# Performance work log

Hardware: AMD Instinct MI355X
Metric: run time of the kernel (lower is better)

## Reference

```python
import jax, jax.numpy as jnp
import numpy as np

# Block-sparse layout constants (must match init_kwargs):
BS = 64       # block_size (= block_m = block_n)
NB = 64       # number of blocks per side -> max_seqlen = 4096
LOCAL = 8     # causal sliding window of 8 blocks
GLOBAL = 1    # 1 global (attention-sink) block


def _layout():
    """Build padded per-row block column indices and the token-level mask.

    Mirrors dkernel semantics: block (i, j) participates iff sparse_pattern[i, j] == 1,
    and within participating blocks a per-token causal mask (k_pos <= q_pos) is applied
    (dkernel applies causal masking on diagonal blocks; off-diagonal lower blocks pass
    the causal test trivially, so pattern & causal is exact).
    """
    i = np.arange(NB)[:, None]
    j = np.arange(NB)[None, :]
    pat = (j <= i) & (((i - j) < LOCAL) | (j < GLOBAL))  # [NB, NB] bool
    max_nnz = int(pat.sum(-1).max())                      # = LOCAL + GLOBAL = 9
    col = np.zeros((NB, max_nnz), np.int32)
    valid = np.zeros((NB, max_nnz), bool)
    for r in range(NB):
        idx = np.nonzero(pat[r])[0]
        col[r, :len(idx)] = idx
        valid[r, :len(idx)] = True
    # token positions
    qpos = np.arange(NB)[:, None] * BS + np.arange(BS)[None, :]                    # [NB, BS]
    kpos = (col[:, :, None] * BS + np.arange(BS)[None, None, :]).reshape(NB, -1)   # [NB, max_nnz*BS]
    vmask = np.repeat(valid, BS, axis=1)                                           # [NB, max_nnz*BS]
    mask = vmask[:, None, :] & (kpos[:, None, :] <= qpos[:, :, None])              # [NB, BS, max_nnz*BS]
    return col, mask

_COL, _MASK = _layout()


def setup_inputs() -> dict:
    key = jax.random.key(0)
    kq, kk, kv = jax.random.split(key, 3)
    B, S, H, D = 2, 4096, 16, 128
    q = jax.random.normal(kq, (B, S, H, D), dtype=jnp.float32)
    k = jax.random.normal(kk, (B, S, H, D), dtype=jnp.float32)
    v = jax.random.normal(kv, (B, S, H, D), dtype=jnp.float32)
    return {"q": q, "k": k, "v": v}


def reference(q, k, v):
    B, S, H, D = q.shape
    sm_scale = 1.0 / np.sqrt(float(D))  # default sm_scale in forward()
    # -> [B, H, NB, BS, D]
    qb = q.reshape(B, NB, BS, H, D).transpose(0, 3, 1, 2, 4)
    kb = k.reshape(B, NB, BS, H, D).transpose(0, 3, 1, 2, 4)
    vb = v.reshape(B, NB, BS, H, D).transpose(0, 3, 1, 2, 4)
    col = jnp.asarray(_COL)                              # [NB, max_nnz]
    # gather the kv blocks each q-block attends to: [B, H, NB, max_nnz*BS, D]
    kg = kb[:, :, col].reshape(B, H, NB, -1, D)
    vg = vb[:, :, col].reshape(B, H, NB, -1, D)
    # block-sparse scores: [B, H, NB, BS, max_nnz*BS]
    s = jnp.einsum('bhnqd,bhnkd->bhnqk', qb, kg) * sm_scale
    s = jnp.where(jnp.asarray(_MASK)[None, None], s, -jnp.inf)
    p = jax.nn.softmax(s, axis=-1)
    o = jnp.einsum('bhnqk,bhnkd->bhnqd', p, vg)          # [B, H, NB, BS, D]
    return o.transpose(0, 2, 3, 1, 4).reshape(B, S, H, D)
```

## Files before the change

### kernel.cpp

```cpp
#include <hip/hip_runtime.h>
#include <hip/hip_bf16.h>


typedef __bf16 bf16_t;
typedef bf16_t bf16x8 __attribute__((ext_vector_type(8)));
typedef bf16_t bf16x4 __attribute__((ext_vector_type(4)));
typedef float f32x4 __attribute__((ext_vector_type(4)));
typedef uint32_t u32x4 __attribute__((ext_vector_type(4)));

#define BSZ 64
#define DIM 128
#define NH 16
#define SEQ 4096
#define ROWSTRIDE (NH * DIM)

__device__ __forceinline__ uint32_t kb_swz(uint32_t A) {
    return A ^ (((A >> 8) & 7u) << 4);
}
__device__ __forceinline__ uint32_t vt_swz(uint32_t A) {
    return A ^ (((A >> 9) & 7u) << 4) ^ (((A >> 8) & 1u) << 6);
}

__global__ __launch_bounds__(256) void sparse_attn_kernel(
    const float* __restrict__ q, const float* __restrict__ k,
    const float* __restrict__ v, float* __restrict__ out)
{
    __shared__ __align__(16) bf16_t Kb[BSZ * DIM];
    __shared__ __align__(16) bf16_t Vt[DIM * BSZ];

    const int L  = ((blockIdx.x & 7) << 8) | (blockIdx.x >> 3);
    const int qi = L & 63;
    const int h  = (L >> 6) & 15;
    const int b  = L >> 10;

    const int tid  = threadIdx.x;
    const int wave = tid >> 6;
    const int lane = tid & 63;
    const int lr = lane & 15;
    const int lk = lane >> 4;
    const int k0 = lk * 8;

    const int sc4 = tid & 31;
    const int sr  = tid >> 5;

    const float scale2 = 0.12751649736230476f;

    const size_t bh_off = ((size_t)b * SEQ * NH + (size_t)h) * DIM;
    const float* kbh = k + bh_off;
    const float* vbh = v + bh_off;

    bf16x8 qf[4];
    {
        const float* qrow = q + bh_off + (size_t)(qi * 64 + wave * 16 + lr) * ROWSTRIDE;
        #pragma unroll
        for (int kk = 0; kk < 4; ++kk) {
            const float4 a0 = *(const float4*)(qrow + 32 * kk + k0);
            const float4 a1 = *(const float4*)(qrow + 32 * kk + k0 + 4);
            bf16x8 f;
            f[0] = (bf16_t)(a0.x * scale2); f[1] = (bf16_t)(a0.y * scale2);
            f[2] = (bf16_t)(a0.z * scale2); f[3] = (bf16_t)(a0.w * scale2);
            f[4] = (bf16_t)(a1.x * scale2); f[5] = (bf16_t)(a1.y * scale2);
            f[6] = (bf16_t)(a1.z * scale2); f[7] = (bf16_t)(a1.w * scale2);
            qf[kk] = f;
        }
    }

    f32x4 oacc[8];
    #pragma unroll
    for (int n = 0; n < 8; ++n) oacc[n] = (f32x4){0.f, 0.f, 0.f, 0.f};
    float mrun = -3.0e38f, lrun = 0.f;

    const int qrow_local = wave * 16 + lr;
    const int nnz = (qi < 8) ? (qi + 1) : 9;

    float4 kreg[8];
    float4 vreg[8];

    #define LOAD_K(jb)                                                            \
    {                                                                             \
        const float* kb_ = kbh + (size_t)((jb) * 64) * ROWSTRIDE + 4 * sc4;       \
        _Pragma("unroll")                                                         \
        for (int i = 0; i < 8; ++i)                                               \
            kreg[i] = *(const float4*)(kb_ + (size_t)(8 * i + sr) * ROWSTRIDE);   \
    }
    #define LOAD_V(jb)                                                            \
    {                                                                             \
        const float* vb_ = vbh + (size_t)((jb) * 64) * ROWSTRIDE + 4 * sc4;       \
        _Pragma("unroll")                                                         \
        for (int T = 0; T < 2; ++T)                                               \
            _Pragma("unroll")                                                     \
            for (int i = 0; i < 4; ++i)                                           \
                vreg[T * 4 + i] = *(const float4*)(vb_ +                          \
                    (size_t)(4 * (sr + 8 * T) + i) * ROWSTRIDE);                  \
    }

    LOAD_K(0);

    for (int t = 0; t < nnz; ++t) {
        const int j = (qi < 8) ? t : ((t == 0) ? 0 : (qi - 8 + t));

        LOAD_V(j);

        #pragma unroll
        for (int i = 0; i < 8; ++i) {
            const float4 t4 = kreg[i];
            bf16x4 c = {(bf16_t)t4.x, (bf16_t)t4.y, (bf16_t)t4.z, (bf16_t)t4.w};
            const uint32_t A = kb_swz((uint32_t)((8 * i + sr) * 256 + 8 * sc4));
            *(bf16x4*)((char*)Kb + A) = c;
        }
        __syncthreads();

        f32x4 sacc[4];
        __builtin_amdgcn_s_setprio(1);
        #pragma unroll
        for (int n = 0; n < 4; ++n) {
            f32x4 a = (f32x4){0.f, 0.f, 0.f, 0.f};
            #pragma unroll
            for (int kk = 0; kk < 4; ++kk) {
                const uint32_t A = kb_swz((uint32_t)((16 * n + lr) * 256 + 64 * kk + 16 * lk));
                bf16x8 kf = *(const bf16x8*)((const char*)Kb + A);
                a = __builtin_amdgcn_mfma_f32_16x16x32_bf16(kf, qf[kk], a, 0, 0, 0);
            }
            sacc[n] = a;
        }
        __builtin_amdgcn_s_setprio(0);

        #pragma unroll
        for (int T = 0; T < 2; ++T) {
            #pragma unroll
            for (int j2 = 0; j2 < 4; ++j2) {
                const int d = 4 * sc4 + j2;
                bf16x4 c = {(bf16_t)((const float*)&vreg[T * 4 + 0])[j2],
                            (bf16_t)((const float*)&vreg[T * 4 + 1])[j2],
                            (bf16_t)((const float*)&vreg[T * 4 + 2])[j2],
                            (bf16_t)((const float*)&vreg[T * 4 + 3])[j2]};
                const uint32_t A = vt_swz((uint32_t)(d * 128 + 8 * (sr + 8 * T)));
                *(bf16x4*)((char*)Vt + A) = c;
            }
        }

        if (j == qi) {
            #pragma unroll
            for (int n = 0; n < 4; ++n)
                #pragma unroll
                for (int r = 0; r < 4; ++r) {
                    if (16 * n + 4 * lk + r > qrow_local) sacc[n][r] = -1.0e30f;
                }
        }
        float vmax = -3.0e38f;
        #pragma unroll
        for (int n = 0; n < 4; ++n)
            #pragma unroll
            for (int r = 0; r < 4; ++r) vmax = fmaxf(vmax, sacc[n][r]);
        vmax = fmaxf(vmax, __shfl_xor(vmax, 16));
        vmax = fmaxf(vmax, __shfl_xor(vmax, 32));

        if (!__all(vmax - mrun <= 8.0f)) {
            const float mnew = fmaxf(mrun, vmax);
            const float alpha = exp2f(mrun - mnew);
            mrun = mnew;
            lrun *= alpha;
            float av[4];
            #pragma unroll
            for (int r = 0; r < 4; ++r) av[r] = __shfl(alpha, 4 * lk + r);
            #pragma unroll
            for (int n = 0; n < 8; ++n)
                #pragma unroll
                for (int r = 0; r < 4; ++r) oacc[n][r] *= av[r];
        }
        uint32_t ch[8];
        #pragma unroll
        for (int n = 0; n < 4; ++n) {
            float p0 = exp2f(sacc[n][0] - mrun);
            float p1 = exp2f(sacc[n][1] - mrun);
            float p2 = exp2f(sacc[n][2] - mrun);
            float p3 = exp2f(sacc[n][3] - mrun);
            lrun += (p0 + p1) + (p2 + p3);
            bf16x4 c4 = {(bf16_t)p0, (bf16_t)p1, (bf16_t)p2, (bf16_t)p3};
            uint32_t* cw = (uint32_t*)&c4;
            ch[2 * n]     = cw[0];
            ch[2 * n + 1] = cw[1];
        }

        bf16x8 paf[2];
        {
            const int s0 = lr + 32 * (lk & 1);
            const bool hi = (lk & 2) != 0;
            #pragma unroll
            for (int kk = 0; kk < 2; ++kk) {
                uint32_t res[4];
                #pragma unroll
                for (int u = 0; u < 2; ++u) {
                    const uint32_t a0 = (uint32_t)__shfl((int)ch[4 * kk + u],     s0);
                    const uint32_t b0 = (uint32_t)__shfl((int)ch[4 * kk + 2 + u], s0);
                    const uint32_t a1 = (uint32_t)__shfl((int)ch[4 * kk + u],     s0 + 16);
                    const uint32_t b1 = (uint32_t)__shfl((int)ch[4 * kk + 2 + u], s0 + 16);
                    res[u]     = hi ? b0 : a0;
                    res[2 + u] = hi ? b1 : a1;
                }
                u32x4 tv = {res[0], res[1], res[2], res[3]};
                paf[kk] = *(bf16x8*)&tv;
            }
        }

        if (t + 1 < nnz) {
            const int jn = (qi < 8) ? (t + 1) : (qi - 8 + t + 1);
            LOAD_K(jn);
        }
        __syncthreads();

        __builtin_amdgcn_s_setprio(1);
        #pragma unroll
        for (int n = 0; n < 8; ++n) {
            f32x4 a = oacc[n];
            #pragma unroll
            for (int kk = 0; kk < 2; ++kk) {
                const uint32_t Av = vt_swz((uint32_t)((16 * n + lr) * 128 + 64 * kk + 16 * lk));
                bf16x8 vf = *(const bf16x8*)((const char*)Vt + Av);
                a = __builtin_amdgcn_mfma_f32_16x16x32_bf16(paf[kk], vf, a, 0, 0, 0);
            }
            oacc[n] = a;
        }
        __builtin_amdgcn_s_setprio(0);
    }

    float lrtot = lrun;
    lrtot += __shfl_xor(lrtot, 16);
    lrtot += __shfl_xor(lrtot, 32);
    float* obase = out + bh_off + (size_t)(qi * 64 + wave * 16) * ROWSTRIDE;
    #pragma unroll
    for (int r = 0; r < 4; ++r) {
        const float inv = 1.0f / __shfl(lrtot, 4 * lk + r);
        float* orow = obase + (size_t)(4 * lk + r) * ROWSTRIDE;
        #pragma unroll
        for (int n = 0; n < 8; ++n) {
            orow[16 * n + lr] = oacc[n][r] * inv;
        }
    }
}

extern "C" void kernel_launch(void* const* d_in, const int* in_sizes, int n_in,
                              void* d_out, int out_size, void* d_ws, size_t ws_size,
                              hipStream_t stream) {
    const float* q = (const float*)d_in[0];
    const float* k = (const float*)d_in[1];
    const float* v = (const float*)d_in[2];
    float* out = (float*)d_out;
    sparse_attn_kernel<<<dim3(2048), dim3(256), 0, stream>>>(q, k, v, out);
}
```

Measured before the change: 105.5 us.

## Process two adjacent query blocks per workgroup to share K/V tile loads

Each workgroup now handles a pair of consecutive query blocks, iterating over the union of their KV windows so each K/V block is loaded from global memory, converted to bf16 and staged in LDS once for both queries. The grid is halved and every MFMA step issues two independent chains. This cuts redundant fp32 K/V traffic and conversion work, but doubles accumulator registers, which may lower occupancy, and halves the number of workgroups available to fill the GPU. The V-transpose swizzle also gains an extra bit.

After: 163.5 us. 54.9% more time.

```diff
diff --git a/kernel.cpp b/kernel.cpp
--- a/kernel.cpp
+++ b/kernel.cpp
@@ -8,7 +8,6 @@
 typedef float f32x4 __attribute__((ext_vector_type(4)));
 typedef uint32_t u32x4 __attribute__((ext_vector_type(4)));
 
-#define BSZ 64
 #define DIM 128
 #define NH 16
 #define SEQ 4096
@@ -18,27 +17,49 @@
     return A ^ (((A >> 8) & 7u) << 4);
 }
 __device__ __forceinline__ uint32_t vt_swz(uint32_t A) {
-    return A ^ (((A >> 9) & 7u) << 4) ^ (((A >> 8) & 1u) << 6);
+    return A ^ (((A >> 9) & 7u) << 4) ^ (((A >> 8) & 1u) << 6) ^ (((A >> 12) & 1u) << 7);
+}
+
+__device__ __forceinline__ void exchange_paf(const uint32_t ch[8], int lr, int lk,
+                                             bf16x8 paf[2]) {
+    const int s0 = lr + 32 * (lk & 1);
+    const bool hi = (lk & 2) != 0;
+    #pragma unroll
+    for (int kk = 0; kk < 2; ++kk) {
+        uint32_t res[4];
+        #pragma unroll
+        for (int u = 0; u < 2; ++u) {
+            const uint32_t a0 = (uint32_t)__shfl((int)ch[4 * kk + u],     s0);
+            const uint32_t b0 = (uint32_t)__shfl((int)ch[4 * kk + 2 + u], s0);
+            const uint32_t a1 = (uint32_t)__shfl((int)ch[4 * kk + u],     s0 + 16);
+            const uint32_t b1 = (uint32_t)__shfl((int)ch[4 * kk + 2 + u], s0 + 16);
+            res[u]     = hi ? b0 : a0;
+            res[2 + u] = hi ? b1 : a1;
+        }
+        u32x4 tv = {res[0], res[1], res[2], res[3]};
+        paf[kk] = *(bf16x8*)&tv;
+    }
 }
 
 __global__ __launch_bounds__(256) void sparse_attn_kernel(
     const float* __restrict__ q, const float* __restrict__ k,
     const float* __restrict__ v, float* __restrict__ out)
 {
-    __shared__ __align__(16) bf16_t Kb[BSZ * DIM];
-    __shared__ __align__(16) bf16_t Vt[DIM * BSZ];
-
-    const int L  = ((blockIdx.x & 7) << 8) | (blockIdx.x >> 3);
-    const int qi = L & 63;
-    const int h  = (L >> 6) & 15;
-    const int b  = L >> 10;
+    __shared__ __align__(16) bf16_t Kb[64 * DIM];
+    __shared__ __align__(16) bf16_t Vt[DIM * 64];
+
+    const int L  = ((blockIdx.x & 7) << 7) | (blockIdx.x >> 3);
+    const int g  = L & 31;
+    const int h  = (L >> 5) & 15;
+    const int b  = L >> 9;
+    const int qiA = 2 * g;
+    const int qiB = 2 * g + 1;
 
     const int tid  = threadIdx.x;
     const int wave = tid >> 6;
     const int lane = tid & 63;
     const int lr = lane & 15;
     const int lk = lane >> 4;
-    const int k0 = lk * 8;
 
     const int sc4 = tid & 31;
     const int sr  = tid >> 5;
@@ -49,29 +70,36 @@
     const float* kbh = k + bh_off;
     const float* vbh = v + bh_off;
 
-    bf16x8 qf[4];
-    {
+    bf16x8 qfA[4], qfB[4];
+    #pragma unroll
+    for (int blk = 0; blk < 2; ++blk) {
+        const int qi = blk ? qiB : qiA;
         const float* qrow = q + bh_off + (size_t)(qi * 64 + wave * 16 + lr) * ROWSTRIDE;
         #pragma unroll
         for (int kk = 0; kk < 4; ++kk) {
-            const float4 a0 = *(const float4*)(qrow + 32 * kk + k0);
-            const float4 a1 = *(const float4*)(qrow + 32 * kk + k0 + 4);
+            const float4 a0 = *(const float4*)(qrow + 32 * kk + 8 * lk);
+            const float4 a1 = *(const float4*)(qrow + 32 * kk + 8 * lk + 4);
             bf16x8 f;
             f[0] = (bf16_t)(a0.x * scale2); f[1] = (bf16_t)(a0.y * scale2);
             f[2] = (bf16_t)(a0.z * scale2); f[3] = (bf16_t)(a0.w * scale2);
             f[4] = (bf16_t)(a1.x * scale2); f[5] = (bf16_t)(a1.y * scale2);
             f[6] = (bf16_t)(a1.z * scale2); f[7] = (bf16_t)(a1.w * scale2);
-            qf[kk] = f;
-        }
-    }
-
-    f32x4 oacc[8];
-    #pragma unroll
-    for (int n = 0; n < 8; ++n) oacc[n] = (f32x4){0.f, 0.f, 0.f, 0.f};
-    float mrun = -3.0e38f, lrun = 0.f;
-
+            if (blk) qfB[kk] = f; else qfA[kk] = f;
+        }
+    }
+
+    f32x4 oA[8], oB[8];
+    #pragma unroll
+    for (int n = 0; n < 8; ++n) {
+        oA[n] = (f32x4){0.f, 0.f, 0.f, 0.f};
+        oB[n] = (f32x4){0.f, 0.f, 0.f, 0.f};
+    }
+    float mrunA = -3.0e38f, lrunA = 0.f;
+    float mrunB = -3.0e38f, lrunB = 0.f;
     const int qrow_local = wave * 16 + lr;
-    const int nnz = (qi < 8) ? (qi + 1) : 9;
+
+    const int lo  = (2 * g - 7 > 1) ? (2 * g - 7) : 1;
+    const int nit = 2 * g + 3 - lo;
 
     float4 kreg[8];
     float4 vreg[8];
@@ -94,10 +122,57 @@
                     (size_t)(4 * (sr + 8 * T) + i) * ROWSTRIDE);                  \
     }
 
+    #define SOFTMAX_EXCH(sX, mrunX, lrunX, oX, pafX, diagX)                       \
+    {                                                                             \
+        if (diagX) {                                                              \
+            _Pragma("unroll")                                                     \
+            for (int n = 0; n < 4; ++n)                                           \
+                _Pragma("unroll")                                                 \
+                for (int r = 0; r < 4; ++r)                                       \
+                    if (16 * n + 4 * lk + r > qrow_local) sX[n][r] = -1.0e30f;    \
+        }                                                                         \
+        float vmax = -3.0e38f;                                                    \
+        _Pragma("unroll")                                                         \
+        for (int n = 0; n < 4; ++n)                                               \
+            _Pragma("unroll")                                                     \
+            for (int r = 0; r < 4; ++r) vmax = fmaxf(vmax, sX[n][r]);             \
+        vmax = fmaxf(vmax, __shfl_xor(vmax, 16));                                 \
+        vmax = fmaxf(vmax, __shfl_xor(vmax, 32));                                 \
+        if (!__all(vmax - mrunX <= 8.0f)) {                                       \
+            const float mnew = fmaxf(mrunX, vmax);                                \
+            const float alpha = exp2f(mrunX - mnew);                              \
+            mrunX = mnew;                                                         \
+            lrunX *= alpha;                                                       \
+            float av[4];                                                          \
+            _Pragma("unroll")                                                     \
+            for (int r = 0; r < 4; ++r) av[r] = __shfl(alpha, 4 * lk + r);        \
+            _Pragma("unroll")                                                     \
+            for (int n = 0; n < 8; ++n)                                           \
+                _Pragma("unroll")                                                 \
+                for (int r = 0; r < 4; ++r) oX[n][r] *= av[r];                    \
+        }                                                                         \
+        uint32_t ch[8];                                                           \
+        _Pragma("unroll")                                                         \
+        for (int n = 0; n < 4; ++n) {                                             \
+            float p0 = exp2f(sX[n][0] - mrunX);                                   \
+            float p1 = exp2f(sX[n][1] - mrunX);                                   \
+            float p2 = exp2f(sX[n][2] - mrunX);                                   \
+            float p3 = exp2f(sX[n][3] - mrunX);                                   \
+            lrunX += (p0 + p1) + (p2 + p3);                                       \
+            bf16x4 c4 = {(bf16_t)p0, (bf16_t)p1, (bf16_t)p2, (bf16_t)p3};         \
+            uint32_t* cw = (uint32_t*)&c4;                                        \
+            ch[2 * n]     = cw[0];                                                \
+            ch[2 * n + 1] = cw[1];                                                \
+        }                                                                         \
+        exchange_paf(ch, lr, lk, pafX);                                           \
+    }
+
     LOAD_K(0);
 
-    for (int t = 0; t < nnz; ++t) {
-        const int j = (qi < 8) ? t : ((t == 0) ? 0 : (qi - 8 + t));
+    for (int t = 0; t < nit; ++t) {
+        const int j = (t == 0) ? 0 : (lo + t - 1);
+        const bool actA = (j == 0) || (j >= qiA - 7 && j <= qiA);
+        const bool actB = (j == 0) || (j >= qiB - 7 && j <= qiB);
 
         LOAD_V(j);
 
@@ -110,18 +185,21 @@
         }
         __syncthreads();
 
-        f32x4 sacc[4];
+        f32x4 sA[4], sB[4];
         __builtin_amdgcn_s_setprio(1);
         #pragma unroll
         for (int n = 0; n < 4; ++n) {
             f32x4 a = (f32x4){0.f, 0.f, 0.f, 0.f};
+            f32x4 c = (f32x4){0.f, 0.f, 0.f, 0.f};
             #pragma unroll
             for (int kk = 0; kk < 4; ++kk) {
                 const uint32_t A = kb_swz((uint32_t)((16 * n + lr) * 256 + 64 * kk + 16 * lk));
                 bf16x8 kf = *(const bf16x8*)((const char*)Kb + A);
-                a = __builtin_amdgcn_mfma_f32_16x16x32_bf16(kf, qf[kk], a, 0, 0, 0);
-            }
-            sacc[n] = a;
+                a = __builtin_amdgcn_mfma_f32_16x16x32_bf16(kf, qfA[kk], a, 0, 0, 0);
+                c = __builtin_amdgcn_mfma_f32_16x16x32_bf16(kf, qfB[kk], c, 0, 0, 0);
+            }
+            sA[n] = a;
+            sB[n] = c;
         }
         __builtin_amdgcn_s_setprio(0);
 
@@ -139,102 +217,46 @@
             }
         }
 
-        if (j == qi) {
-            #pragma unroll
-            for (int n = 0; n < 4; ++n)
-                #pragma unroll
-                for (int r = 0; r < 4; ++r) {
-                    if (16 * n + 4 * lk + r > qrow_local) sacc[n][r] = -1.0e30f;
-                }
-        }
-        float vmax = -3.0e38f;
-        #pragma unroll
-        for (int n = 0; n < 4; ++n)
-            #pragma unroll
-            for (int r = 0; r < 4; ++r) vmax = fmaxf(vmax, sacc[n][r]);
-        vmax = fmaxf(vmax, __shfl_xor(vmax, 16));
-        vmax = fmaxf(vmax, __shfl_xor(vmax, 32));
-
-        if (!__all(vmax - mrun <= 8.0f)) {
-            const float mnew = fmaxf(mrun, vmax);
-            const float alpha = exp2f(mrun - mnew);
-            mrun = mnew;
-            lrun *= alpha;
-            float av[4];
-            #pragma unroll
-            for (int r = 0; r < 4; ++r) av[r] = __shfl(alpha, 4 * lk + r);
-            #pragma unroll
-            for (int n = 0; n < 8; ++n)
-                #pragma unroll
-                for (int r = 0; r < 4; ++r) oacc[n][r] *= av[r];
-        }
-        uint32_t ch[8];
-        #pragma unroll
-        for (int n = 0; n < 4; ++n) {
-            float p0 = exp2f(sacc[n][0] - mrun);
-            float p1 = exp2f(sacc[n][1] - mrun);
-            float p2 = exp2f(sacc[n][2] - mrun);
-            float p3 = exp2f(sacc[n][3] - mrun);
-            lrun += (p0 + p1) + (p2 + p3);
-            bf16x4 c4 = {(bf16_t)p0, (bf16_t)p1, (bf16_t)p2, (bf16_t)p3};
-            uint32_t* cw = (uint32_t*)&c4;
-            ch[2 * n]     = cw[0];
-            ch[2 * n + 1] = cw[1];
-        }
-
-        bf16x8 paf[2];
-        {
-            const int s0 = lr + 32 * (lk & 1);
-            const bool hi = (lk & 2) != 0;
-            #pragma unroll
-            for (int kk = 0; kk < 2; ++kk) {
-                uint32_t res[4];
-                #pragma unroll
-                for (int u = 0; u < 2; ++u) {
-                    const uint32_t a0 = (uint32_t)__shfl((int)ch[4 * kk + u],     s0);
-                    const uint32_t b0 = (uint32_t)__shfl((int)ch[4 * kk + 2 + u], s0);
-                    const uint32_t a1 = (uint32_t)__shfl((int)ch[4 * kk + u],     s0 + 16);
-                    const uint32_t b1 = (uint32_t)__shfl((int)ch[4 * kk + 2 + u], s0 + 16);
-                    res[u]     = hi ? b0 : a0;
-                    res[2 + u] = hi ? b1 : a1;
-                }
-                u32x4 tv = {res[0], res[1], res[2], res[3]};
-                paf[kk] = *(bf16x8*)&tv;
-            }
-        }
-
-        if (t + 1 < nnz) {
-            const int jn = (qi < 8) ? (t + 1) : (qi - 8 + t + 1);
-            LOAD_K(jn);
-        }
+        bf16x8 pafA[2], pafB[2];
+        if (actA) { SOFTMAX_EXCH(sA, mrunA, lrunA, oA, pafA, (j == qiA)); }
+        if (actB) { SOFTMAX_EXCH(sB, mrunB, lrunB, oB, pafB, (j == qiB)); }
+
+        if (t + 1 < nit) { LOAD_K(lo + t); }
         __syncthreads();
 
         __builtin_amdgcn_s_setprio(1);
         #pragma unroll
         for (int n = 0; n < 8; ++n) {
-            f32x4 a = oacc[n];
+            f32x4 a = oA[n];
+            f32x4 c = oB[n];
             #pragma unroll
             for (int kk = 0; kk < 2; ++kk) {
                 const uint32_t Av = vt_swz((uint32_t)((16 * n + lr) * 128 + 64 * kk + 16 * lk));
                 bf16x8 vf = *(const bf16x8*)((const char*)Vt + Av);
-                a = __builtin_amdgcn_mfma_f32_16x16x32_bf16(paf[kk], vf, a, 0, 0, 0);
-            }
-            oacc[n] = a;
+                if (actA) a = __builtin_amdgcn_mfma_f32_16x16x32_bf16(pafA[kk], vf, a, 0, 0, 0);
+                if (actB) c = __builtin_amdgcn_mfma_f32_16x16x32_bf16(pafB[kk], vf, c, 0, 0, 0);
+            }
+            oA[n] = a;
+            oB[n] = c;
         }
         __builtin_amdgcn_s_setprio(0);
     }
 
-    float lrtot = lrun;
-    lrtot += __shfl_xor(lrtot, 16);
-    lrtot += __shfl_xor(lrtot, 32);
-    float* obase = out + bh_off + (size_t)(qi * 64 + wave * 16) * ROWSTRIDE;
-    #pragma unroll
-    for (int r = 0; r < 4; ++r) {
-        const float inv = 1.0f / __shfl(lrtot, 4 * lk + r);
-        float* orow = obase + (size_t)(4 * lk + r) * ROWSTRIDE;
-        #pragma unroll
-        for (int n = 0; n < 8; ++n) {
-            orow[16 * n + lr] = oacc[n][r] * inv;
+    #pragma unroll
+    for (int blk = 0; blk < 2; ++blk) {
+        float lt = blk ? lrunB : lrunA;
+        lt += __shfl_xor(lt, 16);
+        lt += __shfl_xor(lt, 32);
+        const int qi = blk ? qiB : qiA;
+        float* obase = out + bh_off + (size_t)(qi * 64 + wave * 16) * ROWSTRIDE;
+        #pragma unroll
+        for (int r = 0; r < 4; ++r) {
+            const float inv = 1.0f / __shfl(lt, 4 * lk + r);
+            float* orow = obase + (size_t)(4 * lk + r) * ROWSTRIDE;
+            #pragma unroll
+            for (int n = 0; n < 8; ++n) {
+                orow[16 * n + lr] = (blk ? oB[n][r] : oA[n][r]) * inv;
+            }
         }
     }
 }
@@ -246,5 +268,5 @@
     const float* k = (const float*)d_in[1];
     const float* v = (const float*)d_in[2];
     float* out = (float*)d_out;
-    sparse_attn_kernel<<<dim3(2048), dim3(256), 0, stream>>>(q, k, v, out);
-}
+    sparse_attn_kernel<<<dim3(1024), dim3(256), 0, stream>>>(q, k, v, out);
+}
```
